# Kernel tuning notes

Measured on AMD Instinct MI355X. Metric: run time of the kernel, lower is better.

The kernel has to match this reference:

```python
import jax, jax.numpy as jnp
import numpy as np

N_NODES = 327680      # 8192 graphs * 40 nodes/graph
N_EDGES = 2621440     # avg degree 8
NODES_PER_GRAPH = 40


def _lin(k, fan_in, fan_out):
    s = 1.0 / np.sqrt(fan_in)
    return jax.random.uniform(k, (fan_in, fan_out), jnp.float32, -s, s)


def setup_inputs() -> dict:
    key = jax.random.key(0)
    ks = jax.random.split(key, 12)
    x = jax.random.normal(ks[0], (N_NODES, 58), jnp.float32)
    edge_index = jax.random.randint(ks[1], (2, N_EDGES), 0, N_NODES, dtype=jnp.int32)
    return {
        "x": x,
        "edge_index": edge_index,
        "W1": _lin(ks[2], 58, 96),  "b1": jnp.zeros((96,), jnp.float32),
        "W2": _lin(ks[3], 96, 48),  "b2": jnp.zeros((48,), jnp.float32),
        "l1_w": _lin(ks[4], 40 * 48, 256), "l1_b": jnp.zeros((256,), jnp.float32),
        "l2_w": _lin(ks[5], 256, 64),      "l2_b": jnp.zeros((64,), jnp.float32),
        "l3_w": _lin(ks[6], 64, 1),        "l3_b": jnp.zeros((1,), jnp.float32),
    }


def gcn_conv(x, src, dst, W, b, n):
    # PyG GCNConv: h = X W; out[i] = sum_{(j->i)} d_j^-1/2 d_i^-1/2 h[j] + b
    h = x @ W                                   # [N, out]
    deg = jnp.zeros((n,), h.dtype).at[dst].add(1.0)
    dinv = jnp.where(deg > 0, jax.lax.rsqrt(deg), 0.0)
    norm = dinv[src] * dinv[dst]                # [E]
    out = jax.ops.segment_sum(h[src] * norm[:, None], dst, num_segments=n)
    return out + b


def reference(x, edge_index, W1, b1, W2, b2, l1_w, l1_b, l2_w, l2_b, l3_w, l3_b):
    n = x.shape[0]
    loop = jnp.arange(n, dtype=edge_index.dtype)        # self-loops (PyG default)
    src = jnp.concatenate([edge_index[0], loop])
    dst = jnp.concatenate([edge_index[1], loop])
    h = jax.nn.relu(gcn_conv(x, src, dst, W1, b1, n))   # dropout is identity in eval
    h = jax.nn.relu(gcn_conv(h, src, dst, W2, b2, n))
    g = h.reshape(n // NODES_PER_GRAPH, NODES_PER_GRAPH * 48)
    g = jax.nn.relu(g @ l1_w + l1_b)
    g = jax.nn.relu(g @ l2_w + l2_b)
    return jax.nn.sigmoid(g @ l3_w + l3_b)              # [B, 1]
```

## Files before the change

### kernel.cpp

```cpp
#include <hip/hip_runtime.h>

#define N_NODES 327680
#define N_EDGES 2621440
#define NGRAPH  8192
#define NB      640
#define BCAPE   4608

typedef unsigned int uint;
typedef unsigned short u16;
typedef __attribute__((ext_vector_type(8))) short s16x8;
typedef __attribute__((ext_vector_type(4))) float f32x4;

__device__ __forceinline__ float bl(uint u){ return __uint_as_float(u << 16); }
__device__ __forceinline__ float bh(uint u){ return __uint_as_float(u & 0xffff0000u); }
__device__ __forceinline__ u16 f2b(float f){
    uint u = __float_as_uint(f);
    u += 0x7fffu + ((u>>16)&1u);
    return (u16)(u>>16);
}
__device__ __forceinline__ uint pk(float a, float b){
    return (uint)f2b(a) | ((uint)f2b(b) << 16);
}


__device__ void tr_tile(const float* __restrict__ in, u16* __restrict__ out,
                        int K, int N, int Kpad, int kb, int nb){
    __shared__ u16 t[64][72];
    for (int i = threadIdx.x; i < 4096; i += 256){
        int k = i >> 6, n = i & 63;
        int gk = kb + k, gn = nb + n;
        float v = (gk < K && gn < N) ? in[(size_t)gk*N + gn] : 0.f;
        t[n][k] = f2b(v);
    }
    __syncthreads();
    for (int i = threadIdx.x; i < 4096; i += 256){
        int n = i >> 6, k = i & 63;
        int gk = kb + k, gn = nb + n;
        if (gn < N && gk < Kpad) out[(size_t)gn*Kpad + gk] = t[n][k];
    }
}

__global__ __launch_bounds__(256) void k_prep(
    const float* __restrict__ W1, const float* __restrict__ W2,
    const float* __restrict__ l1w, const float* __restrict__ l2w,
    u16* __restrict__ w1t, u16* __restrict__ w2t,
    u16* __restrict__ l1wt, u16* __restrict__ l2wt, int* __restrict__ gcur)
{
    int b = blockIdx.x;
    if (b < 120)      tr_tile(l1w, l1wt, 1920, 256, 1920, (b%30)*64, (b/30)*64);
    else if (b < 124) tr_tile(l2w, l2wt, 256,  64,  256,  (b-120)*64, 0);
    else if (b < 126) tr_tile(W1,  w1t,  58,   96,  64,   0, (b-124)*64);
    else if (b < 128) tr_tile(W2,  w2t,  96,   48,  96,   (b-126)*64, 0);
    else {
        for (int i = threadIdx.x; i < NB; i += 256) gcur[i] = 0;
    }
}


__global__ __launch_bounds__(256) void k_partition(
    const int* __restrict__ src, const int* __restrict__ dst,
    int* __restrict__ gcur, uint* __restrict__ staging)
{
    __shared__ int cnt[NB], base_[NB];
    int tid = threadIdx.x;
    for (int i = tid; i < NB; i += 256) cnt[i] = 0;
    __syncthreads();
    int e0 = blockIdx.x*4096;
    int d[16];
    #pragma unroll
    for (int j = 0; j < 16; ++j){
        d[j] = dst[e0 + j*256 + tid];
        atomicAdd(&cnt[d[j] >> 9], 1);
    }
    __syncthreads();
    for (int i = tid; i < NB; i += 256)
        base_[i] = atomicAdd(&gcur[i], cnt[i]);
    __syncthreads();
    for (int i = tid; i < NB; i += 256) cnt[i] = 0;
    __syncthreads();
    #pragma unroll
    for (int j = 0; j < 16; ++j){
        int e = e0 + j*256 + tid;
        int b = d[j] >> 9;
        int r = atomicAdd(&cnt[b], 1);
        staging[(uint)b*BCAPE + base_[b] + r] = (uint)src[e] | ((uint)(d[j] & 511) << 19);
    }
}


__global__ __launch_bounds__(512) void k_bucket(
    const uint* __restrict__ staging, const int* __restrict__ gcur,
    const float* __restrict__ x,
    int* __restrict__ rowst, int* __restrict__ rendg, float* __restrict__ dinvg,
    int* __restrict__ csr, int* __restrict__ perm, uint* __restrict__ xs32)
{
    __shared__ uint sedge[BCAPE];
    __shared__ int deg[512];
    __shared__ int sc[512];
    __shared__ int cur[512];
    __shared__ int dh[64], dbase[64];
    __shared__ float sdinv[512];
    const int b = blockIdx.x;
    const int tid = threadIdx.x;
    const int lo = b*BCAPE;
    int cnt = gcur[b];
    if (cnt > BCAPE) cnt = BCAPE;
    deg[tid] = 0;
    if (tid < 64) dh[tid] = 0;
    __syncthreads();
    for (int t = tid; t < cnt; t += 512){
        uint ed = staging[lo + t];
        sedge[t] = ed;
        atomicAdd(&deg[ed >> 19], 1);
    }
    __syncthreads();
    int d = deg[tid];
    sc[tid] = d;
    __syncthreads();
    for (int o = 1; o < 512; o <<= 1){
        int v = (tid >= o) ? sc[tid-o] : 0;
        __syncthreads();
        sc[tid] += v;
        __syncthreads();
    }
    int incl = sc[tid];
    int excl = incl - d;
    int gnode = b*512 + tid;
    float dv = 1.0f / sqrtf((float)(d + 1));
    rowst[gnode] = lo + excl;
    rendg[gnode] = lo + incl;
    dinvg[gnode] = dv;
    sdinv[tid] = dv;
    cur[tid] = lo + excl;
    int bin = min(d, 63);
    atomicAdd(&dh[bin], 1);
    __syncthreads();
    if (tid == 0){
        int a = 0;
        #pragma unroll
        for (int i = 0; i < 64; ++i){ dbase[i] = a; a += dh[i]; dh[i] = 0; }
    }
    __syncthreads();
    int pos = dbase[bin] + atomicAdd(&dh[bin], 1);
    perm[b*512 + pos] = gnode;
    for (int t = tid; t < cnt; t += 512){
        uint ed = sedge[t];
        int p = atomicAdd(&cur[ed >> 19], 1);
        csr[p] = (int)(ed & 0x7FFFFu);
    }
    const size_t n0 = (size_t)b*512;
    for (int i = tid; i < 512*32; i += 512){
        int n = i >> 5, c = i & 31;
        float dvn = sdinv[n];
        float a = 0.f, bb = 0.f;
        if (c < 29){
            float2 v = *(const float2*)&x[(n0 + n)*58 + 2*c];
            a = v.x * dvn; bb = v.y * dvn;
        }
        xs32[(n0 + n)*32 + c] = pk(a, bb);
    }
}


__global__ __launch_bounds__(256) void k_fused1(
    const int* __restrict__ rs, const int* __restrict__ re,
    const int* __restrict__ csr, const float* __restrict__ dinv,
    const int* __restrict__ perm,
    const uint4* __restrict__ feat4,
    const u16* __restrict__ w1t,
    const float* __restrict__ b1,
    const u16* __restrict__ w2t,
    u16* __restrict__ ts)
{
    __shared__ __align__(16) u16 As[64][72];
    __shared__ __align__(16) u16 Bt1[96][72];
    __shared__ __align__(16) u16 Bt2[48][104];
    __shared__ __align__(16) u16 sh1[64][104];
    __shared__ float sb1[96];
    __shared__ int   snode[64];
    __shared__ float sdv[64];
    const int tid = threadIdx.x;

    for (int i = tid; i < 768; i += 256){
        int n = i >> 3, s = i & 7;
        *(uint4*)&Bt1[n][s*8] = *(const uint4*)&w1t[n*64 + s*8];
    }
    for (int i = tid; i < 576; i += 256){
        int n = i / 12, s = i % 12;
        *(uint4*)&Bt2[n][s*8] = *(const uint4*)&w2t[n*96 + s*8];
    }
    if (tid < 96) sb1[tid] = b1[tid];

    {
        const int g = tid >> 3, c4 = tid & 7;
        #pragma unroll
        for (int pass = 0; pass < 2; ++pass){
            int row = pass*32 + g;
            int node = perm[blockIdx.x*64 + row];
            float di = dinv[node];
            uint4 u = feat4[((uint)node << 3) + c4];
            float a0 = bl(u.x), a1 = bh(u.x), a2 = bl(u.y), a3 = bh(u.y);
            float a4 = bl(u.z), a5 = bh(u.z), a6 = bl(u.w), a7 = bh(u.w);
            int e = rs[node];
            const int e1 = re[node];
            while (e < e1){
                const int last = e1 - 1;
                int idx[8];
                #pragma unroll
                for (int k = 0; k < 8; ++k) idx[k] = csr[min(e + k, last)];
                uint4 uu[8];
                #pragma unroll
                for (int k = 0; k < 8; ++k) uu[k] = feat4[((uint)idx[k] << 3) + c4];
                #pragma unroll
                for (int k = 0; k < 8; ++k){
                    if (e + k < e1){
                        a0 += bl(uu[k].x); a1 += bh(uu[k].x);
                        a2 += bl(uu[k].y); a3 += bh(uu[k].y);
                        a4 += bl(uu[k].z); a5 += bh(uu[k].z);
                        a6 += bl(uu[k].w); a7 += bh(uu[k].w);
                    }
                }
                e += 8;
            }
            a0 *= di; a1 *= di; a2 *= di; a3 *= di;
            a4 *= di; a5 *= di; a6 *= di; a7 *= di;
            if (c4 == 0){ snode[row] = node; sdv[row] = di; }
            uint4 w;
            w.x = pk(a0,a1); w.y = pk(a2,a3); w.z = pk(a4,a5); w.w = pk(a6,a7);
            *(uint4*)&As[row][c4*8] = w;
        }
    }
    __syncthreads();

    const int wv = tid >> 6, l = tid & 63;
    const int lr = l & 15, lg = l >> 4;
    const int r0 = wv*16;

    f32x4 acc1[6] = {};
    #pragma unroll
    for (int s = 0; s < 2; ++s){
        s16x8 af = *(const s16x8*)&As[r0+lr][s*32 + lg*8];
        #pragma unroll
        for (int t = 0; t < 6; ++t){
            s16x8 bf = *(const s16x8*)&Bt1[t*16+lr][s*32 + lg*8];
            acc1[t] = __builtin_amdgcn_mfma_f32_16x16x32_bf16(af, bf, acc1[t], 0, 0, 0);
        }
    }
    #pragma unroll
    for (int t = 0; t < 6; ++t){
        int col = t*16 + lr;
        float bias = sb1[col];
        #pragma unroll
        for (int r = 0; r < 4; ++r)
            sh1[r0 + lg*4 + r][col] = f2b(fmaxf(acc1[t][r] + bias, 0.f));
    }
    __syncthreads();

    f32x4 acc2[3] = {};
    #pragma unroll
    for (int s = 0; s < 3; ++s){
        s16x8 af = *(const s16x8*)&sh1[r0+lr][s*32 + lg*8];
        #pragma unroll
        for (int t = 0; t < 3; ++t){
            s16x8 bf = *(const s16x8*)&Bt2[t*16+lr][s*32 + lg*8];
            acc2[t] = __builtin_amdgcn_mfma_f32_16x16x32_bf16(af, bf, acc2[t], 0, 0, 0);
        }
    }
    #pragma unroll
    for (int r = 0; r < 4; ++r){
        int row = r0 + lg*4 + r;
        size_t node = (size_t)snode[row];
        float dv = sdv[row];
        #pragma unroll
        for (int t = 0; t < 3; ++t)
            ts[node*48 + t*16 + lr] = f2b(acc2[t][r] * dv);
    }
}


__global__ __launch_bounds__(256) void k_gather2(
    const int* __restrict__ rs, const int* __restrict__ re,
    const int* __restrict__ csr, const float* __restrict__ dinv,
    const int* __restrict__ perm,
    const uint* __restrict__ feat,
    const float* __restrict__ bias,
    uint* __restrict__ out)
{
    int slot = (blockIdx.x*256 + threadIdx.x) >> 3;
    int c4 = threadIdx.x & 7;
    int node = perm[slot];
    uint3 u = *(const uint3*)&feat[(size_t)node*24 + c4*3];
    float a0 = bl(u.x), a1 = bh(u.x), a2 = bl(u.y), a3 = bh(u.y);
    float a4 = bl(u.z), a5 = bh(u.z);
    int e = rs[node];
    const int e1 = re[node];
    while (e < e1){
        const int last = e1 - 1;
        int idx[8];
        #pragma unroll
        for (int k = 0; k < 8; ++k) idx[k] = csr[min(e + k, last)];
        uint3 uu[8];
        #pragma unroll
        for (int k = 0; k < 8; ++k) uu[k] = *(const uint3*)&feat[(size_t)idx[k]*24 + c4*3];
        #pragma unroll
        for (int k = 0; k < 8; ++k){
            if (e + k < e1){
                a0 += bl(uu[k].x); a1 += bh(uu[k].x);
                a2 += bl(uu[k].y); a3 += bh(uu[k].y);
                a4 += bl(uu[k].z); a5 += bh(uu[k].z);
            }
        }
        e += 8;
    }
    float di = dinv[node];
    a0 = fmaxf(a0*di + bias[6*c4+0], 0.f);
    a1 = fmaxf(a1*di + bias[6*c4+1], 0.f);
    a2 = fmaxf(a2*di + bias[6*c4+2], 0.f);
    a3 = fmaxf(a3*di + bias[6*c4+3], 0.f);
    a4 = fmaxf(a4*di + bias[6*c4+4], 0.f);
    a5 = fmaxf(a5*di + bias[6*c4+5], 0.f);
    uint3 w;
    w.x = pk(a0,a1); w.y = pk(a2,a3); w.z = pk(a4,a5);
    *(uint3*)&out[(size_t)node*24 + c4*3] = w;
}


__global__ __launch_bounds__(256) void k_head(
    const u16* __restrict__ A,
    const u16* __restrict__ l1wt,
    const float* __restrict__ l1b,
    const u16* __restrict__ l2wt,
    const float* __restrict__ l2b,
    const float* __restrict__ l3w, const float* __restrict__ l3b,
    float* __restrict__ out)
{
    __shared__ __align__(16) u16 As[32][72];
    __shared__ __align__(16) u16 Bt[256][72];
    __shared__ float part[32][2];
    u16 (*sh1)[264] = (u16(*)[264])&Bt[0][0];
    const int tid = threadIdx.x;
    const int g0 = blockIdx.x*32;
    const int w = tid >> 6, l = tid & 63;
    const int lr = l & 15, lg = l >> 4;
    const int r0 = (w & 1)*16;
    const int c0 = (w >> 1)*128;
    f32x4 acc[8] = {};
    for (int k0 = 0; k0 < 1920; k0 += 64){
        __syncthreads();
        {
            int r = tid >> 3, s = tid & 7;
            *(uint4*)&As[r][s*8] = *(const uint4*)&A[(size_t)(g0+r)*1920 + k0 + s*8];
        }
        for (int i = tid; i < 2048; i += 256){
            int n = i >> 3, s = i & 7;
            *(uint4*)&Bt[n][s*8] = *(const uint4*)&l1wt[(size_t)n*1920 + k0 + s*8];
        }
        __syncthreads();
        #pragma unroll
        for (int s = 0; s < 2; ++s){
            s16x8 af = *(const s16x8*)&As[r0+lr][s*32 + lg*8];
            #pragma unroll
            for (int t = 0; t < 8; ++t){
                s16x8 bf = *(const s16x8*)&Bt[c0 + t*16 + lr][s*32 + lg*8];
                acc[t] = __builtin_amdgcn_mfma_f32_16x16x32_bf16(af, bf, acc[t], 0, 0, 0);
            }
        }
    }
    __syncthreads();
    #pragma unroll
    for (int t = 0; t < 8; ++t){
        int col = c0 + t*16 + lr;
        float bs = l1b[col];
        #pragma unroll
        for (int r = 0; r < 4; ++r)
            sh1[r0 + lg*4 + r][col] = f2b(fmaxf(acc[t][r] + bs, 0.f));
    }
    __syncthreads();
    f32x4 acc2[2] = {};
    #pragma unroll
    for (int s = 0; s < 8; ++s){
        s16x8 af = *(const s16x8*)&sh1[r0+lr][s*32 + lg*8];
        #pragma unroll
        for (int t = 0; t < 2; ++t){
            int col = (w>>1)*32 + t*16 + lr;
            s16x8 bf = *(const s16x8*)&l2wt[(size_t)col*256 + s*32 + lg*8];
            acc2[t] = __builtin_amdgcn_mfma_f32_16x16x32_bf16(af, bf, acc2[t], 0, 0, 0);
        }
    }
    float p[4];
    #pragma unroll
    for (int r = 0; r < 4; ++r){
        p[r] = 0.f;
        #pragma unroll
        for (int t = 0; t < 2; ++t){
            int col = (w>>1)*32 + t*16 + lr;
            p[r] += fmaxf(acc2[t][r] + l2b[col], 0.f) * l3w[col];
        }
    }
    #pragma unroll
    for (int o = 1; o < 16; o <<= 1){
        #pragma unroll
        for (int r = 0; r < 4; ++r) p[r] += __shfl_xor(p[r], o);
    }
    if (lr == 0){
        #pragma unroll
        for (int r = 0; r < 4; ++r)
            part[r0 + lg*4 + r][w>>1] = p[r];
    }
    __syncthreads();
    if (tid < 32)
        out[g0 + tid] = 1.0f / (1.0f + expf(-(part[tid][0] + part[tid][1] + l3b[0])));
}

extern "C" void kernel_launch(void* const* d_in, const int* in_sizes, int n_in,
                              void* d_out, int out_size, void* d_ws, size_t ws_size,
                              hipStream_t stream){
    const float* x   = (const float*)d_in[0];
    const int*   ei  = (const int*)  d_in[1];
    const int*   src = ei;
    const int*   dst = ei + N_EDGES;
    const float* W1  = (const float*)d_in[2];
    const float* b1  = (const float*)d_in[3];
    const float* W2  = (const float*)d_in[4];
    const float* b2  = (const float*)d_in[5];
    const float* l1w = (const float*)d_in[6];
    const float* l1b = (const float*)d_in[7];
    const float* l2w = (const float*)d_in[8];
    const float* l2b = (const float*)d_in[9];
    const float* l3w = (const float*)d_in[10];
    const float* l3b = (const float*)d_in[11];
    float* out = (float*)d_out;

    char* w = (char*)d_ws;
    auto alloc = [&](size_t bytes){ void* p = (void*)w; w += (bytes + 255) & ~(size_t)255; return p; };
    float* dinv    = (float*)alloc((size_t)N_NODES*4);
    int*   rowst   = (int*)  alloc((size_t)N_NODES*4);
    int*   rend    = (int*)  alloc((size_t)N_NODES*4);
    int*   perm    = (int*)  alloc((size_t)N_NODES*4);
    int*   gcur    = (int*)  alloc(NB*4);
    u16*   w1t     = (u16*)  alloc(96*64*2);
    u16*   w2t     = (u16*)  alloc(48*96*2);
    u16*   l1wt    = (u16*)  alloc((size_t)256*1920*2);
    u16*   l2wt    = (u16*)  alloc((size_t)64*256*2);
    int*   csr     = (int*)  alloc((size_t)NB*BCAPE*4);
    uint*  staging = (uint*) alloc((size_t)NB*BCAPE*4);
    uint*  xs32    = (uint*) alloc((size_t)N_NODES*32*4);
    u16*   ts      = (u16*)  alloc((size_t)N_NODES*48*2);
    u16*   agg2    = (u16*)  alloc((size_t)N_NODES*48*2);

    k_prep     <<<129, 256, 0, stream>>>(W1, W2, l1w, l2w, w1t, w2t, l1wt, l2wt, gcur);

    k_partition<<<640, 256, 0, stream>>>(src, dst, gcur, staging);
    k_bucket   <<<640, 512, 0, stream>>>(staging, gcur, x, rowst, rend, dinv, csr, perm, xs32);

    k_fused1   <<<5120, 256, 0, stream>>>(rowst, rend, csr, dinv, perm,
                                          (const uint4*)xs32, w1t, b1, w2t, ts);

    k_gather2  <<<10240, 256, 0, stream>>>(rowst, rend, csr, dinv, perm,
                                           (const uint*)ts, b2, (uint*)agg2);

    k_head     <<<256, 256, 0, stream>>>(agg2, l1wt, l1b, l2wt, l2b, l3w, l3b, out);
}
```

Measured before the change: 351.5 us.

## Split first-layer gather from MFMA MLP and alias intermediate buffers

Measured after the change: 361.4 us. 2.8% more time.

```diff
diff --git a/kernel.cpp b/kernel.cpp
--- a/kernel.cpp
+++ b/kernel.cpp
@@ -162,14 +162,55 @@
 }
 
 
-__global__ __launch_bounds__(256) void k_fused1(
+__global__ __launch_bounds__(256) void k_gather1(
     const int* __restrict__ rs, const int* __restrict__ re,
     const int* __restrict__ csr, const float* __restrict__ dinv,
     const int* __restrict__ perm,
     const uint4* __restrict__ feat4,
+    u16* __restrict__ out)
+{
+    int slot = (blockIdx.x*256 + threadIdx.x) >> 3;
+    int c4 = threadIdx.x & 7;
+    int node = perm[slot];
+    uint4 u = feat4[((uint)node << 3) + c4];
+    float a0 = bl(u.x), a1 = bh(u.x), a2 = bl(u.y), a3 = bh(u.y);
+    float a4 = bl(u.z), a5 = bh(u.z), a6 = bl(u.w), a7 = bh(u.w);
+    int e = rs[node];
+    const int e1 = re[node];
+    while (e < e1){
+        const int last = e1 - 1;
+        int idx[8];
+        #pragma unroll
+        for (int k = 0; k < 8; ++k) idx[k] = csr[min(e + k, last)];
+        uint4 uu[8];
+        #pragma unroll
+        for (int k = 0; k < 8; ++k) uu[k] = feat4[((uint)idx[k] << 3) + c4];
+        #pragma unroll
+        for (int k = 0; k < 8; ++k){
+            if (e + k < e1){
+                a0 += bl(uu[k].x); a1 += bh(uu[k].x);
+                a2 += bl(uu[k].y); a3 += bh(uu[k].y);
+                a4 += bl(uu[k].z); a5 += bh(uu[k].z);
+                a6 += bl(uu[k].w); a7 += bh(uu[k].w);
+            }
+        }
+        e += 8;
+    }
+    float di = dinv[node];
+    a0 *= di; a1 *= di; a2 *= di; a3 *= di;
+    a4 *= di; a5 *= di; a6 *= di; a7 *= di;
+    uint4 w;
+    w.x = pk(a0,a1); w.y = pk(a2,a3); w.z = pk(a4,a5); w.w = pk(a6,a7);
+    *(uint4*)&out[(size_t)node*64 + c4*8] = w;
+}
+
+
+__global__ __launch_bounds__(256) void k_conv_mlp(
+    const u16* __restrict__ A,
     const u16* __restrict__ w1t,
     const float* __restrict__ b1,
     const u16* __restrict__ w2t,
+    const float* __restrict__ dinv,
     u16* __restrict__ ts)
 {
     __shared__ __align__(16) u16 As[64][72];
@@ -177,10 +218,14 @@
     __shared__ __align__(16) u16 Bt2[48][104];
     __shared__ __align__(16) u16 sh1[64][104];
     __shared__ float sb1[96];
-    __shared__ int   snode[64];
-    __shared__ float sdv[64];
     const int tid = threadIdx.x;
-
+    {
+        const u16* Ab = A + (size_t)blockIdx.x*64*64;
+        for (int i = tid; i < 512; i += 256){
+            int r = i >> 3, s = i & 7;
+            *(uint4*)&As[r][s*8] = *(const uint4*)&Ab[r*64 + s*8];
+        }
+    }
     for (int i = tid; i < 768; i += 256){
         int n = i >> 3, s = i & 7;
         *(uint4*)&Bt1[n][s*8] = *(const uint4*)&w1t[n*64 + s*8];
@@ -190,46 +235,6 @@
         *(uint4*)&Bt2[n][s*8] = *(const uint4*)&w2t[n*96 + s*8];
     }
     if (tid < 96) sb1[tid] = b1[tid];
-
-    {
-        const int g = tid >> 3, c4 = tid & 7;
-        #pragma unroll
-        for (int pass = 0; pass < 2; ++pass){
-            int row = pass*32 + g;
-            int node = perm[blockIdx.x*64 + row];
-            float di = dinv[node];
-            uint4 u = feat4[((uint)node << 3) + c4];
-            float a0 = bl(u.x), a1 = bh(u.x), a2 = bl(u.y), a3 = bh(u.y);
-            float a4 = bl(u.z), a5 = bh(u.z), a6 = bl(u.w), a7 = bh(u.w);
-            int e = rs[node];
-            const int e1 = re[node];
-            while (e < e1){
-                const int last = e1 - 1;
-                int idx[8];
-                #pragma unroll
-                for (int k = 0; k < 8; ++k) idx[k] = csr[min(e + k, last)];
-                uint4 uu[8];
-                #pragma unroll
-                for (int k = 0; k < 8; ++k) uu[k] = feat4[((uint)idx[k] << 3) + c4];
-                #pragma unroll
-                for (int k = 0; k < 8; ++k){
-                    if (e + k < e1){
-                        a0 += bl(uu[k].x); a1 += bh(uu[k].x);
-                        a2 += bl(uu[k].y); a3 += bh(uu[k].y);
-                        a4 += bl(uu[k].z); a5 += bh(uu[k].z);
-                        a6 += bl(uu[k].w); a7 += bh(uu[k].w);
-                    }
-                }
-                e += 8;
-            }
-            a0 *= di; a1 *= di; a2 *= di; a3 *= di;
-            a4 *= di; a5 *= di; a6 *= di; a7 *= di;
-            if (c4 == 0){ snode[row] = node; sdv[row] = di; }
-            uint4 w;
-            w.x = pk(a0,a1); w.y = pk(a2,a3); w.z = pk(a4,a5); w.w = pk(a6,a7);
-            *(uint4*)&As[row][c4*8] = w;
-        }
-    }
     __syncthreads();
 
     const int wv = tid >> 6, l = tid & 63;
@@ -266,14 +271,14 @@
             acc2[t] = __builtin_amdgcn_mfma_f32_16x16x32_bf16(af, bf, acc2[t], 0, 0, 0);
         }
     }
+    size_t gbase = (size_t)blockIdx.x*64;
     #pragma unroll
     for (int r = 0; r < 4; ++r){
-        int row = r0 + lg*4 + r;
-        size_t node = (size_t)snode[row];
-        float dv = sdv[row];
+        size_t row = gbase + r0 + lg*4 + r;
+        float dv = dinv[row];
         #pragma unroll
         for (int t = 0; t < 3; ++t)
-            ts[node*48 + t*16 + lr] = f2b(acc2[t][r] * dv);
+            ts[row*48 + t*16 + lr] = f2b(acc2[t][r] * dv);
     }
 }
 
@@ -444,17 +449,22 @@
     u16*   l2wt    = (u16*)  alloc((size_t)64*256*2);
     int*   csr     = (int*)  alloc((size_t)NB*BCAPE*4);
     uint*  staging = (uint*) alloc((size_t)NB*BCAPE*4);
-    uint*  xs32    = (uint*) alloc((size_t)N_NODES*32*4);
-    u16*   ts      = (u16*)  alloc((size_t)N_NODES*48*2);
-    u16*   agg2    = (u16*)  alloc((size_t)N_NODES*48*2);
+    char*  BUF_P   = (char*) alloc((size_t)N_NODES*32*4);
+    char*  BUF_Q   = (char*) alloc((size_t)N_NODES*64*2);
+
+    uint* xs32 = (uint*)BUF_P;
+    u16*  ts   = (u16*) BUF_P;
+    u16*  agg1 = (u16*) BUF_Q;
+    u16*  agg2 = (u16*) BUF_Q;
 
     k_prep     <<<129, 256, 0, stream>>>(W1, W2, l1w, l2w, w1t, w2t, l1wt, l2wt, gcur);
 
     k_partition<<<640, 256, 0, stream>>>(src, dst, gcur, staging);
     k_bucket   <<<640, 512, 0, stream>>>(staging, gcur, x, rowst, rend, dinv, csr, perm, xs32);
 
-    k_fused1   <<<5120, 256, 0, stream>>>(rowst, rend, csr, dinv, perm,
-                                          (const uint4*)xs32, w1t, b1, w2t, ts);
+    k_gather1  <<<10240, 256, 0, stream>>>(rowst, rend, csr, dinv, perm,
+                                           (const uint4*)xs32, agg1);
+    k_conv_mlp <<<5120,  256, 0, stream>>>(agg1, w1t, b1, w2t, dinv, ts);
 
     k_gather2  <<<10240, 256, 0, stream>>>(rowst, rend, csr, dinv, perm,
                                            (const uint*)ts, b2, (uint*)agg2);
```
